# Optimization experiments

Measured on AMD Instinct MI355X. Metric: run time of the kernel, lower is better.

## Reference

```python
import jax, jax.numpy as jnp
import numpy as np

B, S, DIM, HID, E, TOPK = 32, 512, 1024, 4096, 8, 2
CF = 1.0


def setup_inputs() -> dict:
    key = jax.random.key(0)
    ks = jax.random.split(key, 12)
    sc = 0.02
    return {
        "router_input": jax.random.normal(ks[0], (B, S, DIM), jnp.float32),
        "x": jax.random.normal(ks[1], (B, S, DIM), jnp.float32),
        "noise": jax.random.normal(ks[2], (B, E), jnp.float32),
        # router params (stored [in,out])
        "Wg": jax.random.normal(ks[3], (DIM, E), jnp.float32) * sc,
        "bg": jnp.zeros((E,), jnp.float32),
        "Wn": jax.random.normal(ks[4], (DIM, E), jnp.float32) * sc,
        "bn": jnp.zeros((E,), jnp.float32),
        # expert MLP params, stacked over experts
        "W1": jax.random.normal(ks[5], (E, DIM, HID), jnp.float32) * sc,
        "b1": jnp.zeros((E, HID), jnp.float32),
        "W2": jax.random.normal(ks[6], (E, HID, DIM), jnp.float32) * sc,
        "b2": jnp.zeros((E, DIM), jnp.float32),
    }


def reference(router_input, x, noise, Wg, bg, Wn, bn, W1, b1, W2, b2):
    b, s, d = x.shape
    e = Wg.shape[1]
    # ---- noisy top-k router (per-sample: mean over sequence) ----
    ri = router_input.mean(axis=1)                      # [B, D]
    logits = ri @ Wg + bg                               # [B, E]
    noise_logits = ri @ Wn + bn                         # [B, E]
    noisy = logits + noise * jax.nn.softplus(noise_logits)
    top_vals, top_idx = jax.lax.top_k(noisy, TOPK)      # [B, K]
    # softmax over -inf-masked logits == softmax over the kept top-k values
    gate = jax.nn.softmax(top_vals, axis=-1)            # [B, K]

    flat_e = top_idx.reshape(-1)                        # [N] expert id per (sample,k) pair
    flat_w = gate.reshape(-1)                           # [N]
    sample_ids = jnp.repeat(jnp.arange(b), TOPK)        # [N]
    n = b * TOPK
    capacity = max(int(n / e * CF), 1)

    # ---- capacity drop: keep first `capacity` pairs per expert in sorted order ----
    order = jnp.argsort(flat_e, stable=True)            # stable sort by expert id
    sorted_e = flat_e[order]
    rank_in_expert = jnp.arange(n) - jnp.searchsorted(sorted_e, sorted_e, side="left")
    keep = jnp.zeros((n,), bool).at[order].set(rank_in_expert < capacity)

    # ---- per-pair expert MLP via gathered expert weights (grouped GEMM) ----
    xp = x[sample_ids]                                  # [N, S, D]
    h = jnp.einsum("psd,pdh->psh", xp, W1[flat_e]) + b1[flat_e][:, None, :]
    h = jax.nn.gelu(h, approximate=False)               # exact GELU (torch nn.GELU)
    y = jnp.einsum("psh,phd->psd", h, W2[flat_e]) + b2[flat_e][:, None, :]

    # ---- weight by gate, zero dropped pairs, combine back per sample ----
    y = y * (flat_w * keep.astype(y.dtype))[:, None, None]
    return jax.ops.segment_sum(y, sample_ids, num_segments=b)  # [B, S, D]
```

## Files before the change

kernel.cpp:

```cpp
#include <hip/hip_runtime.h>
#include <hip/hip_bf16.h>
#include <math.h>

#define B_    32
#define S_    512
#define DIM_  1024
#define HID_  4096
#define E_    8
#define TOPK_ 2
#define CAP_  8
#define NSLOT_ 64

typedef __bf16 bf16_t;
typedef bf16_t bf16x8 __attribute__((ext_vector_type(8)));
typedef float  f32x4  __attribute__((ext_vector_type(4)));

__device__ __forceinline__ ushort f2bf(float f) {
    union { float f; unsigned u; } v; v.f = f;
    unsigned r = (v.u + 0x7fffu + ((v.u >> 16) & 1u)) >> 16;
    return (ushort)r;
}

__device__ __forceinline__ void async_cp16(const ushort* g, ushort* l) {
    __builtin_amdgcn_global_load_lds(
        (const __attribute__((address_space(1))) unsigned int*)g,
        (__attribute__((address_space(3))) unsigned int*)l, 16, 0, 0);
}

__global__ void k_mean(const float* __restrict__ rin, float* __restrict__ ri) {
    int b = blockIdx.x;
    int d4 = threadIdx.x;
    const float4* p = (const float4*)(rin + (size_t)b * S_ * DIM_) + d4;
    float4 acc = {0.f, 0.f, 0.f, 0.f};
    for (int s = 0; s < S_; ++s) {
        float4 v = p[(size_t)s * (DIM_ / 4)];
        acc.x += v.x; acc.y += v.y; acc.z += v.z; acc.w += v.w;
    }
    const float inv = 1.0f / (float)S_;
    float4 o = {acc.x * inv, acc.y * inv, acc.z * inv, acc.w * inv};
    ((float4*)(ri + (size_t)b * DIM_))[d4] = o;
}

__global__ void k_router(const float* __restrict__ ri, const float* __restrict__ noise,
                         const float* __restrict__ Wg, const float* __restrict__ bg,
                         const float* __restrict__ Wn, const float* __restrict__ bn,
                         int* __restrict__ slot_sample, float* __restrict__ slot_gate) {
    __shared__ float noisy[B_][E_];
    __shared__ int   top_i[B_][TOPK_];
    __shared__ float top_g[B_][TOPK_];
    int t = threadIdx.x;
    int b = t >> 3, e = t & 7;
    {
        float accg = 0.f, accn = 0.f;
        const float* r = ri + (size_t)b * DIM_;
        for (int d = 0; d < DIM_; ++d) {
            float rv = r[d];
            accg += rv * Wg[d * E_ + e];
            accn += rv * Wn[d * E_ + e];
        }
        accg += bg[e]; accn += bn[e];
        float sp = (accn > 20.f) ? accn : log1pf(expf(accn));
        noisy[b][e] = accg + noise[b * E_ + e] * sp;
    }
    __syncthreads();
    if (t < B_) {
        float v1 = -INFINITY, v2 = -INFINITY; int i1 = 0, i2 = 0;
        for (int ee = 0; ee < E_; ++ee) {
            float v = noisy[t][ee];
            if (v > v1)      { v2 = v1; i2 = i1; v1 = v; i1 = ee; }
            else if (v > v2) { v2 = v; i2 = ee; }
        }
        float g2 = expf(v2 - v1);
        float s = 1.f + g2;
        top_i[t][0] = i1; top_i[t][1] = i2;
        top_g[t][0] = 1.f / s; top_g[t][1] = g2 / s;
    }
    if (t < NSLOT_) { slot_sample[t] = -1; slot_gate[t] = 0.f; }
    __syncthreads();
    if (t == 0) {
        int cnt[E_];
        for (int ee = 0; ee < E_; ++ee) cnt[ee] = 0;
        for (int p = 0; p < B_ * TOPK_; ++p) {
            int bb = p >> 1, kk = p & 1;
            int ee = top_i[bb][kk];
            int c = cnt[ee]++;
            if (c < CAP_) {
                slot_sample[ee * CAP_ + c] = bb;
                slot_gate[ee * CAP_ + c]   = top_g[bb][kk];
            }
        }
    }
}

__global__ void k_cvt_x(const float* __restrict__ x, ushort* __restrict__ xb, int n8) {
    int i = blockIdx.x * blockDim.x + threadIdx.x;
    if (i >= n8) return;
    const float4* p = (const float4*)x + (size_t)i * 2;
    float4 a = p[0], b = p[1];
    union { ushort s[8]; uint4 v; } u;
    u.s[0] = f2bf(a.x); u.s[1] = f2bf(a.y); u.s[2] = f2bf(a.z); u.s[3] = f2bf(a.w);
    u.s[4] = f2bf(b.x); u.s[5] = f2bf(b.y); u.s[6] = f2bf(b.z); u.s[7] = f2bf(b.w);
    ((uint4*)xb)[i] = u.v;
}

__global__ void k_transpose_cvt(const float* __restrict__ W, ushort* __restrict__ Wt,
                                int K, int N) {
    __shared__ float tile[64][65];
    size_t eoff = (size_t)blockIdx.z * K * N;
    const float* Win = W + eoff;
    ushort* Wout = Wt + eoff;
    int n0 = blockIdx.x * 64, k0 = blockIdx.y * 64;
    int t = threadIdx.x;
    int r = t >> 4;
    int c4 = (t & 15) << 2;
#pragma unroll
    for (int i = 0; i < 4; ++i) {
        float4 v = *(const float4*)(Win + (size_t)(k0 + r + i * 16) * N + n0 + c4);
        tile[r + i * 16][c4 + 0] = v.x;
        tile[r + i * 16][c4 + 1] = v.y;
        tile[r + i * 16][c4 + 2] = v.z;
        tile[r + i * 16][c4 + 3] = v.w;
    }
    __syncthreads();
#pragma unroll
    for (int i = 0; i < 4; ++i) {
        int nn = r + i * 16;
        ushort4 o;
        o.x = f2bf(tile[c4 + 0][nn]);
        o.y = f2bf(tile[c4 + 1][nn]);
        o.z = f2bf(tile[c4 + 2][nn]);
        o.w = f2bf(tile[c4 + 3][nn]);
        *(ushort4*)(Wout + (size_t)(n0 + nn) * K + k0 + c4) = o;
    }
}

__device__ __forceinline__ void gemm_mainloop(
    const ushort* __restrict__ Abase, int lda,
    const ushort* __restrict__ Bbase, int ldb,
    int K, ushort* lds_a, ushort* lds_b, f32x4 acc[4][4]) {
    int tid = threadIdx.x;
    int wave = tid >> 6, lane = tid & 63;
    int wm = wave & 1, wn = wave >> 1;
    int quad = lane >> 4, mr = lane & 15;
    int r_lo = lane >> 2;
    int kp   = (lane & 3) << 3;
    const ushort* a_g0 = Abase + (size_t)(wave * 16 + r_lo) * lda + kp;
    const ushort* a_g1 = Abase + (size_t)((wave + 4) * 16 + r_lo) * lda + kp;
    const ushort* b_g0 = Bbase + (size_t)(wave * 16 + r_lo) * ldb + kp;
    const ushort* b_g1 = Bbase + (size_t)((wave + 4) * 16 + r_lo) * ldb + kp;
    ushort* a_l0 = lds_a + wave * 512;
    ushort* a_l1 = lds_a + (wave + 4) * 512;
    ushort* b_l0 = lds_b + wave * 512;
    ushort* b_l1 = lds_b + (wave + 4) * 512;
    for (int k0 = 0; k0 < K; k0 += 32) {
        __syncthreads();
        async_cp16(a_g0 + k0, a_l0);
        async_cp16(a_g1 + k0, a_l1);
        async_cp16(b_g0 + k0, b_l0);
        async_cp16(b_g1 + k0, b_l1);
        __syncthreads();
        bf16x8 af[4], bfr[4];
#pragma unroll
        for (int i = 0; i < 4; ++i)
            af[i] = *(const bf16x8*)&lds_a[(wm * 64 + i * 16 + mr) * 32 + quad * 8];
#pragma unroll
        for (int i = 0; i < 4; ++i)
            bfr[i] = *(const bf16x8*)&lds_b[(wn * 64 + i * 16 + mr) * 32 + quad * 8];
#pragma unroll
        for (int i = 0; i < 4; ++i)
#pragma unroll
            for (int j = 0; j < 4; ++j)
                acc[i][j] = __builtin_amdgcn_mfma_f32_16x16x32_bf16(af[i], bfr[j], acc[i][j], 0, 0, 0);
    }
}

__global__ __launch_bounds__(256, 2) void k_gemm1(
    const ushort* __restrict__ xb, const ushort* __restrict__ w1t,
    const float* __restrict__ b1, const int* __restrict__ slot_sample,
    ushort* __restrict__ H) {
    __shared__ ushort As[128 * 32];
    __shared__ ushort Bs[128 * 32];
    int slot = blockIdx.z;
    int samp = slot_sample[slot];
    if (samp < 0) return;
    int e = slot >> 3;
    int mt = blockIdx.y, nt = blockIdx.x;
    const ushort* Abase = xb + ((size_t)samp * S_ + mt * 128) * DIM_;
    const ushort* Bbase = w1t + (size_t)e * HID_ * DIM_ + (size_t)(nt * 128) * DIM_;
    f32x4 acc[4][4];
#pragma unroll
    for (int i = 0; i < 4; ++i)
#pragma unroll
        for (int j = 0; j < 4; ++j) acc[i][j] = (f32x4){0.f, 0.f, 0.f, 0.f};
    gemm_mainloop(Abase, DIM_, Bbase, DIM_, DIM_, As, Bs, acc);
    int wave = threadIdx.x >> 6, lane = threadIdx.x & 63;
    int wm = wave & 1, wn = wave >> 1, quad = lane >> 4, mr = lane & 15;
    ushort* Hrow = H + ((size_t)slot * S_ + mt * 128) * HID_ + nt * 128;
#pragma unroll
    for (int j = 0; j < 4; ++j) {
        int nl = wn * 64 + j * 16 + mr;
        float bias = b1[e * HID_ + nt * 128 + nl];
#pragma unroll
        for (int i = 0; i < 4; ++i) {
#pragma unroll
            for (int r = 0; r < 4; ++r) {
                int ml = wm * 64 + i * 16 + quad * 4 + r;
                float v = acc[i][j][r] + bias;
                float g = 0.5f * v * (1.0f + erff(v * 0.70710678118654752f));
                Hrow[(size_t)ml * HID_ + nl] = f2bf(g);
            }
        }
    }
}

__global__ __launch_bounds__(256, 2) void k_gemm2(
    const ushort* __restrict__ H, const ushort* __restrict__ w2t,
    const float* __restrict__ b2, const int* __restrict__ slot_sample,
    const float* __restrict__ slot_gate, float* __restrict__ out) {
    __shared__ ushort As[128 * 32];
    __shared__ ushort Bs[128 * 32];
    int slot = blockIdx.z;
    int samp = slot_sample[slot];
    if (samp < 0) return;
    int e = slot >> 3;
    float gate = slot_gate[slot];
    int mt = blockIdx.y, nt = blockIdx.x;
    const ushort* Abase = H + ((size_t)slot * S_ + mt * 128) * HID_;
    const ushort* Bbase = w2t + (size_t)e * DIM_ * HID_ + (size_t)(nt * 128) * HID_;
    f32x4 acc[4][4];
#pragma unroll
    for (int i = 0; i < 4; ++i)
#pragma unroll
        for (int j = 0; j < 4; ++j) acc[i][j] = (f32x4){0.f, 0.f, 0.f, 0.f};
    gemm_mainloop(Abase, HID_, Bbase, HID_, HID_, As, Bs, acc);
    int wave = threadIdx.x >> 6, lane = threadIdx.x & 63;
    int wm = wave & 1, wn = wave >> 1, quad = lane >> 4, mr = lane & 15;
    float* Orow = out + ((size_t)samp * S_ + mt * 128) * DIM_ + nt * 128;
#pragma unroll
    for (int j = 0; j < 4; ++j) {
        int nl = wn * 64 + j * 16 + mr;
        float bias = b2[e * DIM_ + nt * 128 + nl];
#pragma unroll
        for (int i = 0; i < 4; ++i) {
#pragma unroll
            for (int r = 0; r < 4; ++r) {
                int ml = wm * 64 + i * 16 + quad * 4 + r;
                float v = acc[i][j][r] + bias;
                atomicAdd(&Orow[(size_t)ml * DIM_ + nl], v * gate);
            }
        }
    }
}

extern "C" void kernel_launch(void* const* d_in, const int* in_sizes, int n_in,
                              void* d_out, int out_size, void* d_ws, size_t ws_size,
                              hipStream_t stream) {
    const float* rin   = (const float*)d_in[0];
    const float* x     = (const float*)d_in[1];
    const float* noise = (const float*)d_in[2];
    const float* Wg    = (const float*)d_in[3];
    const float* bg    = (const float*)d_in[4];
    const float* Wn    = (const float*)d_in[5];
    const float* bn    = (const float*)d_in[6];
    const float* W1    = (const float*)d_in[7];
    const float* b1    = (const float*)d_in[8];
    const float* W2    = (const float*)d_in[9];
    const float* b2    = (const float*)d_in[10];
    float* out = (float*)d_out;

    char* ws = (char*)d_ws;
    float*  ri          = (float*)ws;
    int*    slot_sample = (int*)(ws + 131072);
    float*  slot_gate   = (float*)(ws + 131072 + 256);
    ushort* xb  = (ushort*)(ws + 135168);
    ushort* w1t = (ushort*)(ws + 135168 + 33554432);
    ushort* w2t = (ushort*)(ws + 135168 + 33554432 + 67108864);
    ushort* H   = (ushort*)(ws + 135168 + 33554432 + 2 * 67108864);

    hipMemsetAsync(d_out, 0, (size_t)out_size * sizeof(float), stream);
    k_mean<<<B_, 256, 0, stream>>>(rin, ri);
    k_router<<<1, 256, 0, stream>>>(ri, noise, Wg, bg, Wn, bn, slot_sample, slot_gate);
    k_cvt_x<<<(B_ * S_ * DIM_ / 8 + 255) / 256, 256, 0, stream>>>(x, xb, B_ * S_ * DIM_ / 8);
    k_transpose_cvt<<<dim3(HID_ / 64, DIM_ / 64, E_), 256, 0, stream>>>(W1, w1t, DIM_, HID_);
    k_transpose_cvt<<<dim3(DIM_ / 64, HID_ / 64, E_), 256, 0, stream>>>(W2, w2t, HID_, DIM_);
    k_gemm1<<<dim3(HID_ / 128, S_ / 128, NSLOT_), 256, 0, stream>>>(xb, w1t, b1, slot_sample, H);
    k_gemm2<<<dim3(DIM_ / 128, S_ / 128, NSLOT_), 256, 0, stream>>>(H, w2t, b2, slot_sample, slot_gate, out);
}
```

Baseline: 1.190 ms.

## Remap GEMM grids so each XCD handles one expert; merge weight transposes

Flattens the GEMM grids to 1D and decodes the block id so that blocks landing on the same XCD (round-robin by id mod 8) all work on the same expert. Each expert's weights then stay in that XCD's L2 instead of being spread across all dies. It also raises the launch-bounds occupancy hint from 2 to 4 blocks per CU, which may push up register pressure and cause spills. The two weight-transpose launches are merged into one kernel that picks W1 or W2 from the z index.

```diff
diff --git a/kernel.cpp b/kernel.cpp
--- a/kernel.cpp
+++ b/kernel.cpp
@@ -103,13 +103,20 @@
     ((uint4*)xb)[i] = u.v;
 }
 
-__global__ void k_transpose_cvt(const float* __restrict__ W, ushort* __restrict__ Wt,
-                                int K, int N) {
+__global__ void k_transpose_cvt(const float* __restrict__ W1, ushort* __restrict__ w1t,
+                                const float* __restrict__ W2, ushort* __restrict__ w2t) {
     __shared__ float tile[64][65];
-    size_t eoff = (size_t)blockIdx.z * K * N;
-    const float* Win = W + eoff;
-    ushort* Wout = Wt + eoff;
-    int n0 = blockIdx.x * 64, k0 = blockIdx.y * 64;
+    int z = blockIdx.z;
+    const float* Win; ushort* Wout; int K, N, n0, k0;
+    if (z < 8) {
+        Win = W1 + (size_t)z * DIM_ * HID_; Wout = w1t + (size_t)z * DIM_ * HID_;
+        K = DIM_; N = HID_;
+        n0 = blockIdx.x * 64; k0 = blockIdx.y * 64;
+    } else {
+        Win = W2 + (size_t)(z - 8) * HID_ * DIM_; Wout = w2t + (size_t)(z - 8) * HID_ * DIM_;
+        K = HID_; N = DIM_;
+        n0 = blockIdx.y * 64; k0 = blockIdx.x * 64;
+    }
     int t = threadIdx.x;
     int r = t >> 4;
     int c4 = (t & 15) << 2;
@@ -174,17 +181,23 @@
     }
 }
 
-__global__ __launch_bounds__(256, 2) void k_gemm1(
+__global__ __launch_bounds__(256, 4) void k_gemm1(
     const ushort* __restrict__ xb, const ushort* __restrict__ w1t,
     const float* __restrict__ b1, const int* __restrict__ slot_sample,
     ushort* __restrict__ H) {
     __shared__ ushort As[128 * 32];
     __shared__ ushort Bs[128 * 32];
-    int slot = blockIdx.z;
+    int l = blockIdx.x;
+    int xcd = l & 7;
+    int i0 = l >> 3;
+    int c   = i0 >> 7;
+    int rem = i0 & 127;
+    int mt  = rem >> 5;
+    int nt  = rem & 31;
+    int slot = xcd * 8 + c;
     int samp = slot_sample[slot];
     if (samp < 0) return;
-    int e = slot >> 3;
-    int mt = blockIdx.y, nt = blockIdx.x;
+    int e = xcd;
     const ushort* Abase = xb + ((size_t)samp * S_ + mt * 128) * DIM_;
     const ushort* Bbase = w1t + (size_t)e * HID_ * DIM_ + (size_t)(nt * 128) * DIM_;
     f32x4 acc[4][4];
@@ -213,18 +226,24 @@
     }
 }
 
-__global__ __launch_bounds__(256, 2) void k_gemm2(
+__global__ __launch_bounds__(256, 4) void k_gemm2(
     const ushort* __restrict__ H, const ushort* __restrict__ w2t,
     const float* __restrict__ b2, const int* __restrict__ slot_sample,
     const float* __restrict__ slot_gate, float* __restrict__ out) {
     __shared__ ushort As[128 * 32];
     __shared__ ushort Bs[128 * 32];
-    int slot = blockIdx.z;
+    int l = blockIdx.x;
+    int xcd = l & 7;
+    int i0 = l >> 3;
+    int c   = i0 >> 5;
+    int rem = i0 & 31;
+    int mt  = rem >> 3;
+    int nt  = rem & 7;
+    int slot = xcd * 8 + c;
     int samp = slot_sample[slot];
     if (samp < 0) return;
-    int e = slot >> 3;
+    int e = xcd;
     float gate = slot_gate[slot];
-    int mt = blockIdx.y, nt = blockIdx.x;
     const ushort* Abase = H + ((size_t)slot * S_ + mt * 128) * HID_;
     const ushort* Bbase = w2t + (size_t)e * DIM_ * HID_ + (size_t)(nt * 128) * HID_;
     f32x4 acc[4][4];
@@ -281,8 +300,7 @@
     k_mean<<<B_, 256, 0, stream>>>(rin, ri);
     k_router<<<1, 256, 0, stream>>>(ri, noise, Wg, bg, Wn, bn, slot_sample, slot_gate);
     k_cvt_x<<<(B_ * S_ * DIM_ / 8 + 255) / 256, 256, 0, stream>>>(x, xb, B_ * S_ * DIM_ / 8);
-    k_transpose_cvt<<<dim3(HID_ / 64, DIM_ / 64, E_), 256, 0, stream>>>(W1, w1t, DIM_, HID_);
-    k_transpose_cvt<<<dim3(DIM_ / 64, HID_ / 64, E_), 256, 0, stream>>>(W2, w2t, HID_, DIM_);
-    k_gemm1<<<dim3(HID_ / 128, S_ / 128, NSLOT_), 256, 0, stream>>>(xb, w1t, b1, slot_sample, H);
-    k_gemm2<<<dim3(DIM_ / 128, S_ / 128, NSLOT_), 256, 0, stream>>>(H, w2t, b2, slot_sample, slot_gate, out);
-}
+    k_transpose_cvt<<<dim3(64, 16, 16), 256, 0, stream>>>(W1, w1t, W2, w2t);
+    k_gemm1<<<8192, 256, 0, stream>>>(xb, w1t, b1, slot_sample, H);
+    k_gemm2<<<2048, 256, 0, stream>>>(H, w2t, b2, slot_sample, slot_gate, out);
+}
```

Result: slower. 1.256 ms (+5.5%).
